# Kernel optimization log

Hardware: AMD Instinct MI355X
Metric: run time of the kernel (lower is better)

The kernel has to match this reference:

```python
import jax, jax.numpy as jnp
import numpy as np

STRIDE = 1
PAD = 1

def setup_inputs() -> dict:
    key = jax.random.key(0)
    k1, k2 = jax.random.split(key)
    x = jax.random.normal(k1, (32, 128, 56, 56), dtype=jnp.float32)
    W = jax.random.normal(k2, (256, 128, 3, 3), dtype=jnp.float32)
    b = jnp.zeros((256,), dtype=jnp.float32)
    return {"x": x, "W": W, "b": b}

def reference(x, W, b):
    # Faithful conv2d: NCHW input, OIHW weight, stride 1, pad 1, plus bias.
    out = jax.lax.conv_general_dilated(
        x, W,
        window_strides=(STRIDE, STRIDE),
        padding=((PAD, PAD), (PAD, PAD)),
        dimension_numbers=("NCHW", "OIHW", "NCHW"),
    )
    return out + b[None, :, None, None]
```

## Files before the change

kernel.cpp:

```cpp
#include <hip/hip_runtime.h>
#include <hip/hip_bf16.h>
#include <cstdint>
#include <cstddef>

#define NB   32
#define CIN  128
#define HWP  3136
#define KOC  256
#define NRS  9
#define PROW 3364
#define GUARD 256
#define BEL  8192

typedef __attribute__((ext_vector_type(8))) short  short8;
typedef __attribute__((ext_vector_type(4))) short  short4v;
typedef __attribute__((ext_vector_type(4))) float  float4v;

__device__ __forceinline__ unsigned short f2bf(float f) {
    union { float f; unsigned int u; } v; v.f = f;
    unsigned int u = v.u;
    u = u + 0x7fffu + ((u >> 16) & 1u);
    return (unsigned short)(u >> 16);
}

__global__ __launch_bounds__(256) void prep_kernel(const float* __restrict__ W,
                                                   unsigned short* __restrict__ wt2,
                                                   const float* __restrict__ x,
                                                   unsigned short* __restrict__ xt) {
    __shared__ unsigned short lds[32 * 260];
    int blk = blockIdx.x;
    int t   = threadIdx.x;

    if (blk < 1152) {
        int idx  = blk * 256 + t;
        int e    = idx & 7;
        int lr   = (idx >> 3) & 15;
        int quad = (idx >> 7) & 3;
        int i4   = (idx >> 9) & 3;
        int w4   = (idx >> 11) & 3;
        int q13  = idx >> 13;
        int s    = q13 % 3;
        int r    = (q13 / 3) % 3;
        int ck   = q13 / 9;
        int oc = w4 * 64 + i4 * 16 + lr;
        int c  = ck * 32 + quad * 8 + e;
        wt2[idx] = f2bf(W[((size_t)oc * CIN + c) * NRS + r * 3 + s]);
        return;
    }

    if (blk >= 2816) {
        int g = (blk - 2816) * 256 + t;
        int slab = g / 228;
        int gi   = g - slab * 228;
        int row;
        if (gi < 59)       row = gi;
        else if (gi < 169) { int k = gi - 59;
                             row = 115 + 58 * (k >> 1) + (k & 1); }
        else               row = 3305 + (gi - 169);
        unsigned short* gr = xt + (size_t)slab * (PROW * 32) + (size_t)row * 32;
        short8 z = (short8)0;
        *(short8*)(gr +  0) = z;
        *(short8*)(gr +  8) = z;
        *(short8*)(gr + 16) = z;
        *(short8*)(gr + 24) = z;
        return;
    }

    int b    = blk - 1152;
    int tile = b % 13;
    int ck   = (b / 13) & 3;
    int n    = b / 52;
    int hw0  = tile * 256;
    int wv   = t >> 6;
    int lane = t & 63;

    const float* src = x + ((size_t)(n * CIN + ck * 32)) * HWP;
    #pragma unroll
    for (int pass = 0; pass < 8; ++pass) {
        int c  = pass * 4 + wv;
        int hw = hw0 + lane * 4;
        if (hw < HWP) {
            float4v v = *(const float4v*)(src + (size_t)c * HWP + hw);
            short4v s4;
            #pragma unroll
            for (int k = 0; k < 4; ++k) s4[k] = (short)f2bf(v[k]);
            *(short4v*)(&lds[c * 260 + lane * 4]) = s4;
        }
    }
    __syncthreads();

    int sub = t & 3;
    int hwl = t >> 2;
    unsigned short* dst = xt + ((size_t)(n * 4 + ck)) * PROW * 32;
    #pragma unroll
    for (int pass = 0; pass < 4; ++pass) {
        int hl = pass * 64 + hwl;
        int hw = hw0 + hl;
        if (hw < HWP) {
            short8 v;
            #pragma unroll
            for (int j = 0; j < 8; ++j)
                v[j] = (short)lds[(sub * 8 + j) * 260 + hl];
            int pr = hw + 59 + 2 * (hw / 56);
            *(short8*)(dst + (size_t)pr * 32 + sub * 8) = v;
        }
    }
}

__device__ __forceinline__ void stage_B(const unsigned short* gwin,
                                        unsigned short* lbase,
                                        int wv, int lane) {
    #pragma unroll
    for (int it = 0; it < 4; ++it) {
        int blk = it * 4 + wv;
        int s   = blk * 64 + lane;
        int r   = s >> 2;
        int q   = s & 3;
        int qs  = q ^ ((r >> 1) & 3);
        __builtin_amdgcn_global_load_lds(
            (const __attribute__((address_space(1))) void*)(gwin + r * 32 + qs * 8),
            (__attribute__((address_space(3))) void*)(lbase + (size_t)blk * 512), 16, 0, 0);
    }
}

__device__ __forceinline__ short8 ldb(const char* lb, int r, int quad) {
    int q = quad ^ ((r >> 1) & 3);
    return *(const short8*)(lb + r * 64 + q * 16);
}

__global__ __launch_bounds__(256, 3) void gemm_kernel(const unsigned short* __restrict__ xt,
                                                      const unsigned short* __restrict__ wt2,
                                                      const float* __restrict__ bias,
                                                      float* __restrict__ out) {
    __shared__ unsigned short lds[2 * BEL];

    int bx = blockIdx.x;
    int ot = bx & 1;
    int n  = (bx >> 1) & 31;
    int pt = bx >> 6;
    int p0 = pt * 128;

    int t    = threadIdx.x;
    int wv   = t >> 6;
    int lane = t & 63;
    int lr   = lane & 15;
    int quad = lane >> 4;
    int wm   = wv >> 1;
    int wn   = wv & 1;

    int prbase = p0 + 2 * (p0 / 56);

    int rb[4];
    #pragma unroll
    for (int j = 0; j < 4; ++j) {
        int hw  = p0 + wn * 64 + j * 16 + lr;
        int hwc = hw < HWP ? hw : (HWP - 1);
        rb[j] = hwc + 59 + 2 * (hwc / 56) - prbase;
    }

    const unsigned short* xb = xt + (size_t)n * 4 * PROW * 32;
    const unsigned short* ap = wt2 + (ot * 2 + wm) * 2048 + lane * 8;

    float4v acc[4][4];
    #pragma unroll
    for (int i = 0; i < 4; ++i)
        #pragma unroll
        for (int j = 0; j < 4; ++j)
            acc[i][j] = (float4v){0.f, 0.f, 0.f, 0.f};

    short8 af[12];

    stage_B(xb + (size_t)prbase * 32, lds, wv, lane);
    #pragma unroll
    for (int k = 0; k < 8; ++k)
        af[k] = *(const short8*)(ap + (size_t)(k >> 2) * 8192 + (size_t)(k & 3) * 512);
    __syncthreads();

    for (int ck = 0; ck < 4; ++ck) {
        const char* lbB = (const char*)(lds + (ck & 1) * BEL);
        #pragma unroll
        for (int r = 0; r < 3; ++r) {
            const unsigned short* gb = ap + (size_t)(ck * 9 + r * 3) * 8192;
            int sh0 = (r - 1) * 58;

            #pragma unroll
            for (int s = 0; s < 3; ++s) {
                const int db = 4 * ((s + 2) % 3);
                #pragma unroll
                for (int i = 0; i < 4; ++i)
                    af[db + i] = *(const short8*)(gb + (size_t)(s + 2) * 8192
                                                     + (size_t)i * 512);
                int shift = sh0 + s - 1;
                short8 bcur = ldb(lbB, rb[0] + shift, quad);
                __builtin_amdgcn_s_setprio(1);
                #pragma unroll
                for (int j = 0; j < 4; ++j) {
                    short8 bnext;
                    if (j < 3) bnext = ldb(lbB, rb[j + 1] + shift, quad);
                    #pragma unroll
                    for (int i = 0; i < 4; ++i)
                        acc[i][j] = __builtin_amdgcn_mfma_f32_16x16x32_bf16(
                            af[4 * s + i], bcur, acc[i][j], 0, 0, 0);
                    if (j < 3) bcur = bnext;
                }
                __builtin_amdgcn_s_setprio(0);
            }
        }
        if (ck < 3)
            stage_B(xb + (size_t)(ck + 1) * (PROW * 32) + (size_t)prbase * 32,
                    lds + ((ck + 1) & 1) * BEL, wv, lane);
        __syncthreads();
    }

    float* orow = out + (size_t)n * KOC * HWP;
    #pragma unroll
    for (int i = 0; i < 4; ++i) {
        #pragma unroll
        for (int rr = 0; rr < 4; ++rr) {
            int oc = ot * 128 + wm * 64 + i * 16 + quad * 4 + rr;
            float bi = bias[oc];
            #pragma unroll
            for (int j = 0; j < 4; ++j) {
                int hw = p0 + wn * 64 + j * 16 + lr;
                if (hw < HWP)
                    orow[(size_t)oc * HWP + hw] = acc[i][j][rr] + bi;
            }
        }
    }
}

__global__ void naive_kernel(const float* __restrict__ x, const float* __restrict__ W,
                             const float* __restrict__ b, float* __restrict__ out) {
    size_t idx = (size_t)blockIdx.x * 256 + threadIdx.x;
    if (idx >= (size_t)NB * KOC * HWP) return;
    int w0 = (int)(idx % 56);
    int h0 = (int)((idx / 56) % 56);
    int k  = (int)((idx / HWP) % KOC);
    int n  = (int)(idx / ((size_t)HWP * KOC));
    float acc = b[k];
    for (int c = 0; c < CIN; ++c) {
        const float* xr = x + ((size_t)n * CIN + c) * HWP;
        const float* wr = W + ((size_t)k * CIN + c) * NRS;
        for (int r = 0; r < 3; ++r) {
            int h = h0 + r - 1;
            if ((unsigned)h >= 56u) continue;
            for (int s = 0; s < 3; ++s) {
                int w = w0 + s - 1;
                if ((unsigned)w >= 56u) continue;
                acc += xr[h * 56 + w] * wr[r * 3 + s];
            }
        }
    }
    out[idx] = acc;
}

extern "C" void kernel_launch(void* const* d_in, const int* in_sizes, int n_in,
                              void* d_out, int out_size, void* d_ws, size_t ws_size,
                              hipStream_t stream) {
    const float* x  = (const float*)d_in[0];
    const float* W  = (const float*)d_in[1];
    const float* b  = (const float*)d_in[2];
    float* out = (float*)d_out;

    const size_t wt_elems = (size_t)NRS * 4 * 2 * 2 * 4 * 4 * 16 * 8;
    const size_t xt_elems = (size_t)NB * 4 * PROW * 32 + (size_t)GUARD * 32;
    const size_t need = (wt_elems + xt_elems) * sizeof(unsigned short);

    if (ws_size < need) {
        size_t total = (size_t)NB * KOC * HWP;
        naive_kernel<<<(unsigned)((total + 255) / 256), 256, 0, stream>>>(x, W, b, out);
        return;
    }

    unsigned short* wt2 = (unsigned short*)d_ws;
    unsigned short* xt  = wt2 + wt_elems;

    prep_kernel<<<1152 + NB * 4 * 13 + 114, 256, 0, stream>>>(W, wt2, x, xt);
    gemm_kernel<<<1600, 256, 0, stream>>>(xt, wt2, b, out);
}
```

Before: 238.8 us.

## Reorder weight layout per output tile, remap blocks, and issue B staging earlier

Repacks the bf16 weight buffer so each output-channel tile's weights are contiguous and streamed linearly. The A-fragment prefetch drops from a 3-deep register ring to a 2-deep one. Next-chunk B staging into LDS now starts mid-chunk (r==2, s==0) instead of after all compute, so it overlaps the remaining MFMAs. Block indices are also swizzled so neighbouring workgroups take different image/tile combinations, which may change L2 locality across XCDs. The shallower prefetch could expose more global-load latency on the weight fragments.

Measured after the change: 227.1 us. -4.9%, faster.

```diff
diff --git a/kernel.cpp b/kernel.cpp
--- a/kernel.cpp
+++ b/kernel.cpp
@@ -36,13 +36,16 @@
         int e    = idx & 7;
         int lr   = (idx >> 3) & 15;
         int quad = (idx >> 7) & 3;
-        int i4   = (idx >> 9) & 3;
-        int w4   = (idx >> 11) & 3;
-        int q13  = idx >> 13;
-        int s    = q13 % 3;
-        int r    = (q13 / 3) % 3;
-        int ck   = q13 / 9;
-        int oc = w4 * 64 + i4 * 16 + lr;
+        int i    = (idx >> 9) & 3;
+        int wm   = (idx >> 11) & 1;
+        int q    = idx >> 12;
+        int s    = q % 3;
+        int gg   = q / 3;
+        int g    = gg % 12;
+        int ot   = gg / 12;
+        int ck   = g / 3;
+        int r    = g % 3;
+        int oc = ot * 128 + wm * 64 + i * 16 + lr;
         int c  = ck * 32 + quad * 8 + e;
         wt2[idx] = f2bf(W[((size_t)oc * CIN + c) * NRS + r * 3 + s]);
         return;
@@ -134,11 +137,12 @@
                                                       float* __restrict__ out) {
     __shared__ unsigned short lds[2 * BEL];
 
-    int bx = blockIdx.x;
-    int ot = bx & 1;
-    int n  = (bx >> 1) & 31;
-    int pt = bx >> 6;
-    int p0 = pt * 128;
+    int bx0 = blockIdx.x;
+    int bx  = (bx0 & 7) * 200 + (bx0 >> 3);
+    int ot  = bx & 1;
+    int n   = (bx >> 1) & 31;
+    int pt  = bx >> 6;
+    int p0  = pt * 128;
 
     int t    = threadIdx.x;
     int wv   = t >> 6;
@@ -158,8 +162,8 @@
         rb[j] = hwc + 59 + 2 * (hwc / 56) - prbase;
     }
 
-    const unsigned short* xb = xt + (size_t)n * 4 * PROW * 32;
-    const unsigned short* ap = wt2 + (ot * 2 + wm) * 2048 + lane * 8;
+    const unsigned short* xb  = xt + (size_t)n * 4 * PROW * 32;
+    const unsigned short* agp = wt2 + ot * 147456 + wm * 2048 + lane * 8;
 
     float4v acc[4][4];
     #pragma unroll
@@ -168,28 +172,28 @@
         for (int j = 0; j < 4; ++j)
             acc[i][j] = (float4v){0.f, 0.f, 0.f, 0.f};
 
-    short8 af[12];
+    short8 af_cur[4], af_nxt[4];
 
     stage_B(xb + (size_t)prbase * 32, lds, wv, lane);
     #pragma unroll
-    for (int k = 0; k < 8; ++k)
-        af[k] = *(const short8*)(ap + (size_t)(k >> 2) * 8192 + (size_t)(k & 3) * 512);
+    for (int i = 0; i < 4; ++i)
+        af_cur[i] = *(const short8*)(agp + i * 512);
     __syncthreads();
 
     for (int ck = 0; ck < 4; ++ck) {
         const char* lbB = (const char*)(lds + (ck & 1) * BEL);
         #pragma unroll
         for (int r = 0; r < 3; ++r) {
-            const unsigned short* gb = ap + (size_t)(ck * 9 + r * 3) * 8192;
             int sh0 = (r - 1) * 58;
-
             #pragma unroll
             for (int s = 0; s < 3; ++s) {
-                const int db = 4 * ((s + 2) % 3);
                 #pragma unroll
                 for (int i = 0; i < 4; ++i)
-                    af[db + i] = *(const short8*)(gb + (size_t)(s + 2) * 8192
-                                                     + (size_t)i * 512);
+                    af_nxt[i] = *(const short8*)(agp + 4096 + i * 512);
+                if (r == 2 && s == 0 && ck < 3)
+                    stage_B(xb + (size_t)(ck + 1) * (PROW * 32) + (size_t)prbase * 32,
+                            lds + ((ck + 1) & 1) * BEL, wv, lane);
+
                 int shift = sh0 + s - 1;
                 short8 bcur = ldb(lbB, rb[0] + shift, quad);
                 __builtin_amdgcn_s_setprio(1);
@@ -200,15 +204,15 @@
                     #pragma unroll
                     for (int i = 0; i < 4; ++i)
                         acc[i][j] = __builtin_amdgcn_mfma_f32_16x16x32_bf16(
-                            af[4 * s + i], bcur, acc[i][j], 0, 0, 0);
+                            af_cur[i], bcur, acc[i][j], 0, 0, 0);
                     if (j < 3) bcur = bnext;
                 }
                 __builtin_amdgcn_s_setprio(0);
+                #pragma unroll
+                for (int i = 0; i < 4; ++i) af_cur[i] = af_nxt[i];
+                agp += 4096;
             }
         }
-        if (ck < 3)
-            stage_B(xb + (size_t)(ck + 1) * (PROW * 32) + (size_t)prbase * 32,
-                    lds + ((ck + 1) & 1) * BEL, wv, lane);
         __syncthreads();
     }
 
```
